# Kernel tuning notes

Measured on AMD Instinct MI355X. Metric: run time of the kernel, lower is better.

## Reference

```python
import jax, jax.numpy as jnp
import numpy as np

D_MODEL = 1024
N_HEADS = 16
D_K = D_MODEL // N_HEADS
NEG_INF = -1.0e9


def setup_inputs() -> dict:
    key = jax.random.key(0)
    ks = jax.random.split(key, 12)
    B, S = 2, 2048
    inp = {
        "q": jax.random.normal(ks[0], (B, S, D_MODEL), dtype=jnp.float32),
        "k": jax.random.normal(ks[1], (B, S, D_MODEL), dtype=jnp.float32),
        "v": jax.random.normal(ks[2], (B, S, D_MODEL), dtype=jnp.float32),
        "mask": jax.random.randint(ks[3], (B, 1, S, S), 0, 2, dtype=jnp.int32),
        "Wq": jax.random.normal(ks[4], (D_MODEL, D_MODEL), dtype=jnp.float32) / np.sqrt(D_MODEL),
        "bq": jnp.zeros((D_MODEL,), dtype=jnp.float32),
        "Wk": jax.random.normal(ks[5], (D_MODEL, D_MODEL), dtype=jnp.float32) / np.sqrt(D_MODEL),
        "bk": jnp.zeros((D_MODEL,), dtype=jnp.float32),
        "Wv": jax.random.normal(ks[6], (D_MODEL, D_MODEL), dtype=jnp.float32) / np.sqrt(D_MODEL),
        "bv": jnp.zeros((D_MODEL,), dtype=jnp.float32),
        "Wo": jax.random.normal(ks[7], (D_MODEL, D_MODEL), dtype=jnp.float32) / np.sqrt(D_MODEL),
        "bo": jnp.zeros((D_MODEL,), dtype=jnp.float32),
    }
    return inp


def _split_heads(x):
    B, S, _ = x.shape
    return x.reshape(B, S, N_HEADS, D_K).transpose(0, 2, 1, 3)  # [B,H,S,Dk]


def reference(q, k, v, mask, Wq, bq, Wk, bk, Wv, bv, Wo, bo):
    # QKV projections (nn.Linear: x @ W.T + b; here W stored as [in,out]-agnostic square)
    query = _split_heads(q @ Wq + bq)
    key_ = _split_heads(k @ Wk + bk)
    value = _split_heads(v @ Wv + bv)

    scale = 1.0 / np.sqrt(D_K).astype(np.float32)
    scores = jnp.einsum("bhqd,bhkd->bhqk", query, key_) * scale  # [B,H,S,S]
    scores = jnp.where(mask == 0, NEG_INF, scores)
    attn = jax.nn.softmax(scores, axis=-1)  # dropout is identity in eval (p=0.0)
    ctx = jnp.einsum("bhqk,bhkd->bhqd", attn, value)  # [B,H,S,Dk]

    B, H, S, Dk = ctx.shape
    ctx = ctx.transpose(0, 2, 1, 3).reshape(B, S, H * Dk)
    return ctx @ Wo + bo
```

## Files before the change

### kernel.cpp

```cpp
#include <hip/hip_runtime.h>
#include <hip/hip_bf16.h>

typedef __bf16 bf16_t;
typedef __bf16 bf16x2 __attribute__((ext_vector_type(2)));
typedef __bf16 bf16x8 __attribute__((ext_vector_type(8)));
typedef float f32x4 __attribute__((ext_vector_type(4)));
typedef float f32x16 __attribute__((ext_vector_type(16)));
typedef int intx4 __attribute__((ext_vector_type(4)));
typedef unsigned int u32;
typedef unsigned long long u64;

#define S_LEN 2048
#define DM 1024
#define NH 16
#define DK 64
#define M_ROWS 4096
#define SCALE_LOG2E 0.1803368801111204f

__device__ __forceinline__ int sw_off(int row, int col) {
  return row * 64 + ((((col >> 3) ^ row) & 7) << 3) + (col & 7);
}

__device__ __forceinline__ bf16x8 cvt8(const float4& a, const float4& b) {
  bf16x8 v;
  v[0] = (__bf16)a.x; v[1] = (__bf16)a.y; v[2] = (__bf16)a.z; v[3] = (__bf16)a.w;
  v[4] = (__bf16)b.x; v[5] = (__bf16)b.y; v[6] = (__bf16)b.z; v[7] = (__bf16)b.w;
  return v;
}

__device__ __forceinline__ void glds16(const bf16_t* g, bf16_t* l) {
  __builtin_amdgcn_global_load_lds(
      (const __attribute__((address_space(1))) void*)g,
      (__attribute__((address_space(3))) void*)l, 16, 0, 0);
}

__device__ __forceinline__ int pk2(float lo, float hi) {
  bf16x2 t;
  t[0] = (__bf16)lo;
  t[1] = (__bf16)hi;
  return __builtin_bit_cast(int, t);
}

__global__ __launch_bounds__(256) void pack_mask(
    const int* __restrict__ mask, u64* __restrict__ mb)
{
  const int wgl = blockIdx.x * 4 + (threadIdx.x >> 6);
  const int lane = threadIdx.x & 63;
  const int q = wgl & 2047;
  const int kw = (wgl >> 11) & 31;
  const int b = wgl >> 16;
  const int val = mask[((size_t)(b * S_LEN + q)) * S_LEN + kw * 64 + lane];
  const u64 bits = __ballot(val != 0);
  if (lane == 0) mb[wgl] = bits;
}

__global__ __launch_bounds__(256) void cvt_inputs(
    const float* __restrict__ q, const float* __restrict__ k,
    const float* __restrict__ v, bf16_t* __restrict__ Xb)
{
  const int z = blockIdx.y;
  const float* __restrict__ src = (z == 0) ? q : ((z == 1) ? k : v);
  const size_t idx = ((size_t)blockIdx.x * 256 + threadIdx.x) * 8;
  const float4 a = *(const float4*)&src[idx];
  const float4 b = *(const float4*)&src[idx + 4];
  *(bf16x8*)&Xb[(size_t)z * M_ROWS * DM + idx] = cvt8(a, b);
}

__global__ __launch_bounds__(256) void transw_kernel(
    const float* __restrict__ Wq, const float* __restrict__ Wk,
    const float* __restrict__ Wv, const float* __restrict__ Wo,
    bf16_t* __restrict__ Wt)
{
  const int z = blockIdx.z;
  const float* __restrict__ W = (z == 0) ? Wq : ((z == 1) ? Wk : ((z == 2) ? Wv : Wo));
  bf16_t* __restrict__ out = Wt + (size_t)z * DM * DM;
  __shared__ float tile[64][65];
  const int tx = threadIdx.x & 31, ty = threadIdx.x >> 5;
  const int k0 = blockIdx.x * 64, n0 = blockIdx.y * 64;
  #pragma unroll
  for (int j = 0; j < 8; ++j) {
    const float2 v = *(const float2*)&W[(size_t)(k0 + ty + 8 * j) * DM + n0 + tx * 2];
    tile[ty + 8 * j][tx * 2] = v.x;
    tile[ty + 8 * j][tx * 2 + 1] = v.y;
  }
  __syncthreads();
  #pragma unroll
  for (int j = 0; j < 8; ++j) {
    const int a = ty + 8 * j;
    bf16x2 p;
    p[0] = (__bf16)tile[tx * 2][a];
    p[1] = (__bf16)tile[tx * 2 + 1][a];
    *(bf16x2*)&out[(size_t)(n0 + a) * DM + k0 + tx * 2] = p;
  }
}

__device__ __forceinline__ void gemm128_body(
    const bf16_t* __restrict__ A, const bf16_t* __restrict__ Bt,
    const float* __restrict__ bias, const float scale,
    bf16_t* __restrict__ outb, float* __restrict__ outf)
{
  __shared__ __align__(16) bf16_t As[128 * 32];
  __shared__ __align__(16) bf16_t Bs[128 * 32];
  const int t = threadIdx.x, w = t >> 6, L = t & 63, quad = L >> 4, l16 = L & 15;
  const int m0 = blockIdx.x * 128, n0 = blockIdx.y * 128;
  const int mb = 64 * (w & 1), nb = 64 * (w >> 1);
  const int rowS = t >> 2, subS = (t & 3) * 8;

  f32x4 acc[4][4] = {};
  for (int k0 = 0; k0 < DM; k0 += 32) {
    __syncthreads();
    glds16(&A[(size_t)(m0 + rowS) * DM + k0 + subS],        &As[t * 8]);
    glds16(&A[(size_t)(m0 + 64 + rowS) * DM + k0 + subS],   &As[2048 + t * 8]);
    glds16(&Bt[(size_t)(n0 + rowS) * DM + k0 + subS],       &Bs[t * 8]);
    glds16(&Bt[(size_t)(n0 + 64 + rowS) * DM + k0 + subS],  &Bs[2048 + t * 8]);
    __syncthreads();
    bf16x8 af[4], bfr[4];
    #pragma unroll
    for (int mt = 0; mt < 4; ++mt)
      af[mt] = *(const bf16x8*)&As[(mb + 16 * mt + l16) * 32 + quad * 8];
    #pragma unroll
    for (int ct = 0; ct < 4; ++ct)
      bfr[ct] = *(const bf16x8*)&Bs[(nb + 16 * ct + l16) * 32 + quad * 8];
    #pragma unroll
    for (int mt = 0; mt < 4; ++mt)
      #pragma unroll
      for (int ct = 0; ct < 4; ++ct)
        acc[mt][ct] = __builtin_amdgcn_mfma_f32_16x16x32_bf16(af[mt], bfr[ct], acc[mt][ct], 0, 0, 0);
  }
  #pragma unroll
  for (int mt = 0; mt < 4; ++mt)
    #pragma unroll
    for (int ct = 0; ct < 4; ++ct)
      #pragma unroll
      for (int r = 0; r < 4; ++r) {
        const int row = m0 + mb + 16 * mt + quad * 4 + r;
        const int n = n0 + nb + 16 * ct + l16;
        const float val = (acc[mt][ct][r] + bias[n]) * scale;
        if (outb) outb[(size_t)row * DM + n] = (__bf16)val;
        else      outf[(size_t)row * DM + n] = val;
      }
}

__global__ __launch_bounds__(256) void gemm_qkv(
    const bf16_t* __restrict__ Xb, const bf16_t* __restrict__ Wt,
    const float* __restrict__ bq, const float* __restrict__ bk,
    const float* __restrict__ bv, bf16_t* __restrict__ QKVb)
{
  const int z = blockIdx.z;
  gemm128_body(Xb + (size_t)z * M_ROWS * DM, Wt + (size_t)z * DM * DM,
               (z == 0) ? bq : ((z == 1) ? bk : bv),
               (z == 0) ? SCALE_LOG2E : 1.0f,
               QKVb + (size_t)z * M_ROWS * DM, nullptr);
}

__global__ __launch_bounds__(256) void gemm_out(
    const bf16_t* __restrict__ ctx, const bf16_t* __restrict__ Wto,
    const float* __restrict__ bo, float* __restrict__ out)
{
  gemm128_body(ctx, Wto, bo, 1.0f, nullptr, out);
}

__global__ __launch_bounds__(256) void transpV(
    const bf16_t* __restrict__ Vb, bf16_t* __restrict__ Vtw)
{
  __shared__ bf16_t Tr[64 * 72];
  const int t = threadIdx.x;
  const int key0 = blockIdx.x * 64;
  const int bh = blockIdx.y, b = bh >> 4, h = bh & 15;
  const int r = t >> 2, c = (t & 3) * 16;
  const bf16_t* src = &Vb[(size_t)(b * S_LEN + key0 + r) * DM + h * DK + c];
  const bf16x8 v0 = *(const bf16x8*)src;
  const bf16x8 v1 = *(const bf16x8*)(src + 8);
  #pragma unroll
  for (int j = 0; j < 8; ++j) {
    Tr[r * 72 + c + j] = v0[j];
    Tr[r * 72 + c + 8 + j] = v1[j];
  }
  __syncthreads();
  const int dv = t >> 2, kc = (t & 3) * 16;
  bf16_t ov[16];
  #pragma unroll
  for (int j = 0; j < 16; ++j) ov[j] = Tr[(kc + j) * 72 + dv];
  bf16_t* dst = &Vtw[((size_t)bh * DK + dv) * S_LEN + key0 + kc];
  *(bf16x8*)dst = *(bf16x8*)&ov[0];
  *(bf16x8*)(dst + 8) = *(bf16x8*)&ov[8];
}

__global__ __launch_bounds__(256, 4) void attn_kernel(
    const bf16_t* __restrict__ Qb, const bf16_t* __restrict__ Kb,
    const bf16_t* __restrict__ Vtw, const u64* __restrict__ mb,
    bf16_t* __restrict__ ctx)
{
  __shared__ __align__(16) bf16_t Qs[64 * 64];
  __shared__ __align__(16) bf16_t KVs[4][64 * 64];

  const int t = threadIdx.x, w = t >> 6, L = t & 63;
  const int l31 = L & 31, h5 = L >> 5;
  const int qhalf = w & 1, khalf = w >> 1;
  const int q0 = blockIdx.x * 64;
  const int bh = blockIdx.y, b = bh >> 4, h = bh & 15;
  const int sr = t >> 2, sc = (t & 3) * 16;

  {
    const bf16_t* s = &Qb[(size_t)(b * S_LEN + q0 + sr) * DM + h * DK + sc];
    *(bf16x8*)&Qs[sw_off(sr, sc)]     = *(const bf16x8*)s;
    *(bf16x8*)&Qs[sw_off(sr, sc + 8)] = *(const bf16x8*)(s + 8);
  }
  __syncthreads();

  bf16x8 qf[4];
  #pragma unroll
  for (int ks = 0; ks < 4; ++ks)
    qf[ks] = *(const bf16x8*)&Qs[sw_off(32 * qhalf + l31, ks * 16 + 8 * h5)];

  bf16x8 onesf;
  #pragma unroll
  for (int i = 0; i < 8; ++i) onesf[i] = (__bf16)1.0f;

  const int ch = (L & 7) ^ (L >> 3);
  const int row0 = w * 16 + (L >> 3);
  const int kofs0 = w * 1024 + L * 8, kofs1 = kofs0 + 512;
  const bf16_t* pK0 = &Kb[(size_t)(b * S_LEN + row0) * DM + h * DK + ch * 8];
  const bf16_t* pK1 = pK0 + (size_t)8 * DM;
  const bf16_t* pV0 = &Vtw[((size_t)bh * DK + row0) * S_LEN + ch * 8];
  const bf16_t* pV1 = pV0 + (size_t)8 * S_LEN;

  const int qg = q0 + 32 * qhalf + l31;
  const u64* pm = &mb[(size_t)b * 32 * S_LEN + qg];

  auto stageKV = [&](int buf) {
    glds16(pK0, &KVs[buf][kofs0]);
    glds16(pK1, &KVs[buf][kofs1]);
    glds16(pV0, &KVs[2 + buf][kofs0]);
    glds16(pV1, &KVs[2 + buf][kofs1]);
    pK0 += (size_t)64 * DM; pK1 += (size_t)64 * DM;
    pV0 += 64; pV1 += 64;
  };

  f32x16 O[2] = {};
  f32x16 l_acc = {};

  auto compute = [&](int buf, u64 mcur) {
    const bf16_t* __restrict__ Kc = &KVs[buf][0];
    const bf16_t* __restrict__ Vc = &KVs[2 + buf][0];
    f32x16 sacc = {};
    __builtin_amdgcn_s_setprio(1);
    #pragma unroll
    for (int ks = 0; ks < 4; ++ks) {
      const bf16x8 kf = *(const bf16x8*)&Kc[sw_off(khalf * 32 + l31, ks * 16 + 8 * h5)];
      sacc = __builtin_amdgcn_mfma_f32_32x32x16_bf16(kf, qf[ks], sacc, 0, 0, 0);
    }
    __builtin_amdgcn_s_setprio(0);
    const u32 mm = ((u32)(mcur >> (khalf ? 32 : 0))) >> (4 * h5);
    float p[16];
    #pragma unroll
    for (int r = 0; r < 16; ++r) {
      const int cb = (r & 3) + 8 * (r >> 2);
      const u32 mr = (u32)(((int)(mm << (31 - cb))) >> 31);
      const float e = __builtin_exp2f(sacc[r]);
      p[r] = __builtin_bit_cast(float, __builtin_bit_cast(u32, e) & mr);
    }
    #pragma unroll
    for (int ss = 0; ss < 2; ++ss) {
      const int x0 = pk2(p[8 * ss + 0], p[8 * ss + 1]);
      const int x1 = pk2(p[8 * ss + 2], p[8 * ss + 3]);
      const int y0 = pk2(p[8 * ss + 4], p[8 * ss + 5]);
      const int y1 = pk2(p[8 * ss + 6], p[8 * ss + 7]);
      const auto r0 = __builtin_amdgcn_permlane32_swap(x0, y0, false, false);
      const auto r1 = __builtin_amdgcn_permlane32_swap(x1, y1, false, false);
      intx4 wv;
      wv[0] = r0[0]; wv[1] = r1[0]; wv[2] = r0[1]; wv[3] = r1[1];
      const bf16x8 pf = __builtin_bit_cast(bf16x8, wv);
      const int s4 = 2 * khalf + ss;
      __builtin_amdgcn_s_setprio(1);
      l_acc = __builtin_amdgcn_mfma_f32_32x32x16_bf16(onesf, pf, l_acc, 0, 0, 0);
      #pragma unroll
      for (int ot = 0; ot < 2; ++ot) {
        const bf16x8 vf = *(const bf16x8*)&Vc[sw_off(32 * ot + l31, s4 * 16 + 8 * h5)];
        O[ot] = __builtin_amdgcn_mfma_f32_32x32x16_bf16(vf, pf, O[ot], 0, 0, 0);
      }
      __builtin_amdgcn_s_setprio(0);
    }
  };

  stageKV(0);
  u64 mcur = *pm; pm += S_LEN;
  u64 mnext;
  __syncthreads();

  for (int kt = 0; kt < S_LEN / 64; kt += 2) {
    stageKV(1);
    mnext = *pm; pm += S_LEN;
    compute(0, mcur);
    __syncthreads();
    mcur = mnext;
    if (kt + 2 < S_LEN / 64) {
      stageKV(0);
      mnext = *pm; pm += S_LEN;
    }
    compute(1, mcur);
    __syncthreads();
    mcur = mnext;
  }

  const float lw = l_acc[0];
  float* Osc = (float*)&KVs[0][0];
  float* Lsc = Osc + 4096;
  if (khalf == 1) {
    #pragma unroll
    for (int ot = 0; ot < 2; ++ot)
      #pragma unroll
      for (int r = 0; r < 16; ++r) {
        const int dv = 32 * ot + (r & 3) + 8 * (r >> 2) + 4 * h5;
        Osc[qhalf * 2048 + dv * 32 + l31] = O[ot][r];
      }
    if (h5 == 0) Lsc[qhalf * 32 + l31] = lw;
  }
  __syncthreads();
  if (khalf == 0) {
    const float inv = 1.f / (lw + Lsc[qhalf * 32 + l31]);
    #pragma unroll
    for (int ot = 0; ot < 2; ++ot)
      #pragma unroll
      for (int r = 0; r < 16; ++r) {
        const int dv = 32 * ot + (r & 3) + 8 * (r >> 2) + 4 * h5;
        const float val = (O[ot][r] + Osc[qhalf * 2048 + dv * 32 + l31]) * inv;
        Qs[sw_off(32 * qhalf + l31, dv)] = (__bf16)val;
      }
    const int erow = 32 * qhalf + (L >> 1);
    const int ecol = (L & 1) * 32;
    bf16_t* dst = &ctx[(size_t)(b * S_LEN + q0 + erow) * DM + h * DK + ecol];
    #pragma unroll
    for (int c8 = 0; c8 < 4; ++c8)
      *(bf16x8*)(dst + 8 * c8) = *(const bf16x8*)&Qs[sw_off(erow, ecol + 8 * c8)];
  }
}

extern "C" void kernel_launch(void* const* d_in, const int* in_sizes, int n_in,
                              void* d_out, int out_size, void* d_ws, size_t ws_size,
                              hipStream_t stream) {
  const float* q  = (const float*)d_in[0];
  const float* k  = (const float*)d_in[1];
  const float* v  = (const float*)d_in[2];
  const int* mask = (const int*)d_in[3];
  const float* Wq = (const float*)d_in[4];
  const float* bq = (const float*)d_in[5];
  const float* Wk = (const float*)d_in[6];
  const float* bk = (const float*)d_in[7];
  const float* Wv = (const float*)d_in[8];
  const float* bv = (const float*)d_in[9];
  const float* Wo = (const float*)d_in[10];
  const float* bo = (const float*)d_in[11];
  float* out = (float*)d_out;

  const size_t SLICE = (size_t)M_ROWS * DM;
  bf16_t* Xb   = (bf16_t*)d_ws;
  bf16_t* QKVb = Xb + 3 * SLICE;
  bf16_t* Wt   = QKVb + 3 * SLICE;
  u64* mbw     = (u64*)(Wt + (size_t)4 * DM * DM);
  bf16_t* ctx  = Xb;
  bf16_t* Vtw  = Xb + SLICE;

  pack_mask<<<dim3(32768), dim3(256), 0, stream>>>(mask, mbw);
  cvt_inputs<<<dim3(2048, 3), dim3(256), 0, stream>>>(q, k, v, Xb);
  transw_kernel<<<dim3(16, 16, 4), dim3(256), 0, stream>>>(Wq, Wk, Wv, Wo, Wt);
  gemm_qkv<<<dim3(32, 8, 3), dim3(256), 0, stream>>>(Xb, Wt, bq, bk, bv, QKVb);
  transpV<<<dim3(32, 32), dim3(256), 0, stream>>>(QKVb + 2 * SLICE, Vtw);
  attn_kernel<<<dim3(32, 32), dim3(256), 0, stream>>>(QKVb, QKVb + SLICE, Vtw, mbw, ctx);
  gemm_out<<<dim3(32, 8), dim3(256), 0, stream>>>(ctx, Wt + (size_t)3 * DM * DM, bo, out);
}
```

Measured before the change: 290.8 us.

## Load K/V fragments directly from global memory instead of LDS double-buffering

Removes the shared-memory K/V double buffer and its per-tile barriers. Each wave now loads its K and transposed-V MFMA fragments straight from global memory into registers every key tile. LDS now only holds the Q tile and the final reduction scratch, and launch bounds drop from 4 to 2 blocks per CU. This trades barrier and LDS traffic for uncached or poorly coalesced global loads that are not software-prefetched, so load latency may be exposed.

```diff
diff --git a/kernel.cpp b/kernel.cpp
--- a/kernel.cpp
+++ b/kernel.cpp
@@ -186,13 +186,13 @@
   *(bf16x8*)(dst + 8) = *(bf16x8*)&ov[8];
 }
 
-__global__ __launch_bounds__(256, 4) void attn_kernel(
+__global__ __launch_bounds__(256, 2) void attn_kernel(
     const bf16_t* __restrict__ Qb, const bf16_t* __restrict__ Kb,
     const bf16_t* __restrict__ Vtw, const u64* __restrict__ mb,
     bf16_t* __restrict__ ctx)
 {
   __shared__ __align__(16) bf16_t Qs[64 * 64];
-  __shared__ __align__(16) bf16_t KVs[4][64 * 64];
+  __shared__ float Osc[2 * 2048 + 64];
 
   const int t = threadIdx.x, w = t >> 6, L = t & 63;
   const int l31 = L & 31, h5 = L >> 5;
@@ -217,94 +217,65 @@
   #pragma unroll
   for (int i = 0; i < 8; ++i) onesf[i] = (__bf16)1.0f;
 
-  const int ch = (L & 7) ^ (L >> 3);
-  const int row0 = w * 16 + (L >> 3);
-  const int kofs0 = w * 1024 + L * 8, kofs1 = kofs0 + 512;
-  const bf16_t* pK0 = &Kb[(size_t)(b * S_LEN + row0) * DM + h * DK + ch * 8];
-  const bf16_t* pK1 = pK0 + (size_t)8 * DM;
-  const bf16_t* pV0 = &Vtw[((size_t)bh * DK + row0) * S_LEN + ch * 8];
-  const bf16_t* pV1 = pV0 + (size_t)8 * S_LEN;
+  const bf16_t* kb = &Kb[(size_t)(b * S_LEN + khalf * 32 + l31) * DM + h * DK + 8 * h5];
+  const bf16_t* vb0 = &Vtw[((size_t)bh * DK + l31) * S_LEN + 8 * h5];
+  const bf16_t* vb1 = vb0 + (size_t)32 * S_LEN;
 
   const int qg = q0 + 32 * qhalf + l31;
   const u64* pm = &mb[(size_t)b * 32 * S_LEN + qg];
 
-  auto stageKV = [&](int buf) {
-    glds16(pK0, &KVs[buf][kofs0]);
-    glds16(pK1, &KVs[buf][kofs1]);
-    glds16(pV0, &KVs[2 + buf][kofs0]);
-    glds16(pV1, &KVs[2 + buf][kofs1]);
-    pK0 += (size_t)64 * DM; pK1 += (size_t)64 * DM;
-    pV0 += 64; pV1 += 64;
-  };
-
   f32x16 O[2] = {};
   f32x16 l_acc = {};
-
-  auto compute = [&](int buf, u64 mcur) {
-    const bf16_t* __restrict__ Kc = &KVs[buf][0];
-    const bf16_t* __restrict__ Vc = &KVs[2 + buf][0];
+  const int msh = khalf ? 32 : 0;
+
+  for (int kt = 0; kt < S_LEN / 64; ++kt) {
+    const u64 mcur = *pm; pm += S_LEN;
+    const bf16x8 kf0 = *(const bf16x8*)(kb + 0);
+    const bf16x8 kf1 = *(const bf16x8*)(kb + 16);
+    const bf16x8 kf2 = *(const bf16x8*)(kb + 32);
+    const bf16x8 kf3 = *(const bf16x8*)(kb + 48);
     f32x16 sacc = {};
     __builtin_amdgcn_s_setprio(1);
-    #pragma unroll
-    for (int ks = 0; ks < 4; ++ks) {
-      const bf16x8 kf = *(const bf16x8*)&Kc[sw_off(khalf * 32 + l31, ks * 16 + 8 * h5)];
-      sacc = __builtin_amdgcn_mfma_f32_32x32x16_bf16(kf, qf[ks], sacc, 0, 0, 0);
-    }
+    sacc = __builtin_amdgcn_mfma_f32_32x32x16_bf16(kf0, qf[0], sacc, 0, 0, 0);
+    sacc = __builtin_amdgcn_mfma_f32_32x32x16_bf16(kf1, qf[1], sacc, 0, 0, 0);
+    sacc = __builtin_amdgcn_mfma_f32_32x32x16_bf16(kf2, qf[2], sacc, 0, 0, 0);
+    sacc = __builtin_amdgcn_mfma_f32_32x32x16_bf16(kf3, qf[3], sacc, 0, 0, 0);
     __builtin_amdgcn_s_setprio(0);
-    const u32 mm = ((u32)(mcur >> (khalf ? 32 : 0))) >> (4 * h5);
-    float p[16];
+
+    const u32 mm = ((u32)(mcur >> msh)) >> (4 * h5);
     #pragma unroll
     for (int r = 0; r < 16; ++r) {
       const int cb = (r & 3) + 8 * (r >> 2);
       const u32 mr = (u32)(((int)(mm << (31 - cb))) >> 31);
       const float e = __builtin_exp2f(sacc[r]);
-      p[r] = __builtin_bit_cast(float, __builtin_bit_cast(u32, e) & mr);
+      sacc[r] = __builtin_bit_cast(float, __builtin_bit_cast(u32, e) & mr);
     }
     #pragma unroll
     for (int ss = 0; ss < 2; ++ss) {
-      const int x0 = pk2(p[8 * ss + 0], p[8 * ss + 1]);
-      const int x1 = pk2(p[8 * ss + 2], p[8 * ss + 3]);
-      const int y0 = pk2(p[8 * ss + 4], p[8 * ss + 5]);
-      const int y1 = pk2(p[8 * ss + 6], p[8 * ss + 7]);
+      const int x0 = pk2(sacc[8 * ss + 0], sacc[8 * ss + 1]);
+      const int x1 = pk2(sacc[8 * ss + 2], sacc[8 * ss + 3]);
+      const int y0 = pk2(sacc[8 * ss + 4], sacc[8 * ss + 5]);
+      const int y1 = pk2(sacc[8 * ss + 6], sacc[8 * ss + 7]);
       const auto r0 = __builtin_amdgcn_permlane32_swap(x0, y0, false, false);
       const auto r1 = __builtin_amdgcn_permlane32_swap(x1, y1, false, false);
       intx4 wv;
       wv[0] = r0[0]; wv[1] = r1[0]; wv[2] = r0[1]; wv[3] = r1[1];
       const bf16x8 pf = __builtin_bit_cast(bf16x8, wv);
       const int s4 = 2 * khalf + ss;
+      const bf16x8 vf0 = *(const bf16x8*)(vb0 + s4 * 16);
+      const bf16x8 vf1 = *(const bf16x8*)(vb1 + s4 * 16);
       __builtin_amdgcn_s_setprio(1);
       l_acc = __builtin_amdgcn_mfma_f32_32x32x16_bf16(onesf, pf, l_acc, 0, 0, 0);
-      #pragma unroll
-      for (int ot = 0; ot < 2; ++ot) {
-        const bf16x8 vf = *(const bf16x8*)&Vc[sw_off(32 * ot + l31, s4 * 16 + 8 * h5)];
-        O[ot] = __builtin_amdgcn_mfma_f32_32x32x16_bf16(vf, pf, O[ot], 0, 0, 0);
-      }
+      O[0] = __builtin_amdgcn_mfma_f32_32x32x16_bf16(vf0, pf, O[0], 0, 0, 0);
+      O[1] = __builtin_amdgcn_mfma_f32_32x32x16_bf16(vf1, pf, O[1], 0, 0, 0);
       __builtin_amdgcn_s_setprio(0);
     }
-  };
-
-  stageKV(0);
-  u64 mcur = *pm; pm += S_LEN;
-  u64 mnext;
-  __syncthreads();
-
-  for (int kt = 0; kt < S_LEN / 64; kt += 2) {
-    stageKV(1);
-    mnext = *pm; pm += S_LEN;
-    compute(0, mcur);
-    __syncthreads();
-    mcur = mnext;
-    if (kt + 2 < S_LEN / 64) {
-      stageKV(0);
-      mnext = *pm; pm += S_LEN;
-    }
-    compute(1, mcur);
-    __syncthreads();
-    mcur = mnext;
+    kb += (size_t)64 * DM;
+    vb0 += 64;
+    vb1 += 64;
   }
 
   const float lw = l_acc[0];
-  float* Osc = (float*)&KVs[0][0];
   float* Lsc = Osc + 4096;
   if (khalf == 1) {
     #pragma unroll
```

Result: slower. 345.4 us (+18.8%).
